# Optimization experiments

Hardware: AMD Instinct MI355X
Metric: run time of the kernel (lower is better)

Reference implementation:

```python
import jax, jax.numpy as jnp
import numpy as np

N_NODES = 50000
N_EDGES = 500000
NEG_SLOPE = 0.2


def gat_conv(h, src, dst, W, attn_l, attn_r, bias, activation):
    """DGL-style GATConv (feat_drop=attn_drop=0, no residual).
    h: [N, F_in]; W: [F_in, H*D]; attn_l/attn_r: [H, D]; bias: [H*D].
    Returns [N, H, D]."""
    H, D = attn_l.shape
    feat = (h @ W).reshape(-1, H, D)                      # [N, H, D]
    el = (feat * attn_l).sum(-1)                          # [N, H]
    er = (feat * attn_r).sum(-1)                          # [N, H]
    e = jax.nn.leaky_relu(el[src] + er[dst], NEG_SLOPE)   # [E, H] edge logits
    # edge softmax over incoming edges of each dst node
    emax = jax.ops.segment_max(e, dst, num_segments=N_NODES)
    emax = jnp.where(jnp.isfinite(emax), emax, 0.0)       # guard zero in-degree
    ee = jnp.exp(e - emax[dst])                           # [E, H]
    denom = jax.ops.segment_sum(ee, dst, num_segments=N_NODES)
    alpha = ee / jnp.maximum(denom[dst], 1e-9)            # [E, H]
    # weighted scatter-aggregate of source features
    out = jax.ops.segment_sum(feat[src] * alpha[..., None], dst,
                              num_segments=N_NODES)       # [N, H, D]
    out = out + bias.reshape(1, H, D)
    return activation(out) if activation is not None else out


def setup_inputs() -> dict:
    key = jax.random.key(0)
    ks = jax.random.split(key, 20)
    in0, in1, hid, heads, ncls = 256, 128, 64, 8, 10

    def xn(k, shape):
        fan = shape[0] + (shape[1] if len(shape) > 1 else shape[0])
        return jax.random.normal(k, shape, jnp.float32) * np.float32(np.sqrt(2.0 / fan)) * 1.414

    inp = {
        "feat0": jax.random.normal(ks[0], (30000, in0), jnp.float32),
        "feat1": jax.random.normal(ks[1], (20000, in1), jnp.float32),
        "fc0_w": xn(ks[2], (in0, hid)), "fc0_b": jnp.zeros((hid,), jnp.float32),
        "fc1_w": xn(ks[3], (in1, hid)), "fc1_b": jnp.zeros((hid,), jnp.float32),
        "W0": xn(ks[4], (hid, heads * hid)),
        "al0": xn(ks[5], (heads, hid)), "ar0": xn(ks[6], (heads, hid)),
        "b0": jnp.zeros((heads * hid,), jnp.float32),
        "W1": xn(ks[7], (heads * hid, heads * hid)),
        "al1": xn(ks[8], (heads, hid)), "ar1": xn(ks[9], (heads, hid)),
        "b1": jnp.zeros((heads * hid,), jnp.float32),
        "W2": xn(ks[10], (heads * hid, 1 * ncls)),
        "al2": xn(ks[11], (1, ncls)), "ar2": xn(ks[12], (1, ncls)),
        "b2": jnp.zeros((ncls,), jnp.float32),
        "edge_index": jax.random.randint(ks[13], (2, N_EDGES), 0, N_NODES, jnp.int64
                                         if jax.config.jax_enable_x64 else jnp.int32),
    }
    return inp


def reference(feat0, feat1, fc0_w, fc0_b, fc1_w, fc1_b,
              W0, al0, ar0, b0, W1, al1, ar1, b1, W2, al2, ar2, b2,
              edge_index):
    src, dst = edge_index[0], edge_index[1]
    # per-type linear projection then concat along node axis
    h = jnp.concatenate([feat0 @ fc0_w + fc0_b, feat1 @ fc1_w + fc1_b], axis=0)
    h = gat_conv(h, src, dst, W0, al0, ar0, b0, jax.nn.elu).reshape(N_NODES, -1)
    h = gat_conv(h, src, dst, W1, al1, ar1, b1, jax.nn.elu).reshape(N_NODES, -1)
    logits = gat_conv(h, src, dst, W2, al2, ar2, b2, None).mean(axis=1)  # [N, ncls]
    return logits
```

## Files before the change

kernel.cpp:

```cpp
#include <hip/hip_runtime.h>
#include <hip/hip_bf16.h>
#include <hip/hip_fp16.h>

#define N_NODES 50000
#define N_EDGES 500000
#define HEADS 8
#define HID 64
#define HD 512
#define NCLS 10
#define M_PAD 50048

typedef _Float16 f16x8 __attribute__((ext_vector_type(8)));
typedef _Float16 h8v   __attribute__((ext_vector_type(8)));
typedef float    f32x4 __attribute__((ext_vector_type(4)));

#define GLD_LDS16(g, l) __builtin_amdgcn_global_load_lds( \
    (__attribute__((address_space(1))) void*)(g),         \
    (__attribute__((address_space(3))) void*)(l), 16, 0, 0)

#define T0_TILES 469
#define T1_TILES 313
__global__ __launch_bounds__(256) void fc_gemm(const float* __restrict__ A0,
                                               const float* __restrict__ B0,
                                               const float* __restrict__ bias0,
                                               const float* __restrict__ A1,
                                               const float* __restrict__ B1,
                                               const float* __restrict__ bias1,
                                               _Float16* __restrict__ Cb) {
    __shared__ float As[16][68];
    __shared__ float Bs[16][68];
    int bid = blockIdx.x;
    const float* A; const float* B; const float* bias;
    int M, K, row_off, m0;
    if (bid < T0_TILES) { A = A0; B = B0; bias = bias0; M = 30000; K = 256; row_off = 0;     m0 = bid * 64; }
    else                { A = A1; B = B1; bias = bias1; M = 20000; K = 128; row_off = 30000; m0 = (bid - T0_TILES) * 64; }
    int tid = threadIdx.x;
    int tx = tid & 15, ty = tid >> 4;
    float acc[4][4] = {};
    int arow = tid >> 2;
    int akq  = (tid & 3) * 4;
    int brow = tid >> 4;
    int bcol = (tid & 15) * 4;
    for (int k0 = 0; k0 < K; k0 += 16) {
        int m = m0 + arow;
        float4 av = make_float4(0.f, 0.f, 0.f, 0.f);
        if (m < M) av = *(const float4*)(A + (size_t)m * K + k0 + akq);
        As[akq + 0][arow] = av.x; As[akq + 1][arow] = av.y;
        As[akq + 2][arow] = av.z; As[akq + 3][arow] = av.w;
        float4 bv = *(const float4*)(B + (size_t)(k0 + brow) * 64 + bcol);
        *(float4*)(&Bs[brow][bcol]) = bv;
        __syncthreads();
#pragma unroll
        for (int k = 0; k < 16; k++) {
            float4 a = *(const float4*)(&As[k][ty * 4]);
            float4 b = *(const float4*)(&Bs[k][tx * 4]);
            float av4[4] = {a.x, a.y, a.z, a.w};
            float bv4[4] = {b.x, b.y, b.z, b.w};
#pragma unroll
            for (int i = 0; i < 4; i++)
#pragma unroll
                for (int j = 0; j < 4; j++) acc[i][j] += av4[i] * bv4[j];
        }
        __syncthreads();
    }
#pragma unroll
    for (int i = 0; i < 4; i++) {
        int m = m0 + ty * 4 + i;
        if (m < M) {
#pragma unroll
            for (int j = 0; j < 4; j++) {
                int col = tx * 4 + j;
                Cb[(size_t)(row_off + m) * 64 + col] = (_Float16)(acc[i][j] + bias[col]);
            }
        }
    }
}

#define NBLK_SCAN 196

__global__ void count_kernel(const int* __restrict__ dst, int* __restrict__ cnt) {
    int t = blockIdx.x * blockDim.x + threadIdx.x;
    if (t < N_EDGES) atomicAdd(&cnt[dst[t]], 1);
}

__global__ void scan_part(const int* __restrict__ cnt, int* __restrict__ part) {
    __shared__ int s[256];
    int i = blockIdx.x * 256 + threadIdx.x;
    s[threadIdx.x] = (i < N_NODES) ? cnt[i] : 0;
    __syncthreads();
    for (int off = 128; off; off >>= 1) {
        if (threadIdx.x < off) s[threadIdx.x] += s[threadIdx.x + off];
        __syncthreads();
    }
    if (threadIdx.x == 0) part[blockIdx.x] = s[0];
}

__global__ void scan_offs(int* __restrict__ part) {
    __shared__ int s[256];
    int tid = threadIdx.x;
    int v = (tid < NBLK_SCAN) ? part[tid] : 0;
    s[tid] = v;
    __syncthreads();
    for (int off = 1; off < 256; off <<= 1) {
        int x = (tid >= off) ? s[tid - off] : 0;
        __syncthreads();
        s[tid] += x;
        __syncthreads();
    }
    if (tid < NBLK_SCAN) part[tid] = s[tid] - v;
}

__global__ void scan_apply(const int* __restrict__ cnt, const int* __restrict__ part,
                           int* __restrict__ rp, int* __restrict__ cur) {
    __shared__ int s[256];
    int tid = threadIdx.x;
    int i = blockIdx.x * 256 + tid;
    int v = (i < N_NODES) ? cnt[i] : 0;
    s[tid] = v;
    __syncthreads();
    for (int off = 1; off < 256; off <<= 1) {
        int x = (tid >= off) ? s[tid - off] : 0;
        __syncthreads();
        s[tid] += x;
        __syncthreads();
    }
    if (i < N_NODES) {
        int excl = s[tid] - v + part[blockIdx.x];
        rp[i] = excl; cur[i] = excl;
    }
    if (i == 0) rp[N_NODES] = N_EDGES;
}

__global__ void scatter_kernel(const int* __restrict__ src, const int* __restrict__ dst,
                               int* __restrict__ cursor, int* __restrict__ src_sorted) {
    int t = blockIdx.x * blockDim.x + threadIdx.x;
    if (t >= N_EDGES) return;
    int pos = atomicAdd(&cursor[dst[t]], 1);
    src_sorted[pos] = src[t];
}

__global__ void wtrans(const float* __restrict__ W0, const float* __restrict__ W1,
                       _Float16* __restrict__ W0t, _Float16* __restrict__ W1t) {
    int t = blockIdx.x * blockDim.x + threadIdx.x;
    if (t < 64 * 512) {
        int n = t >> 6, k = t & 63;
        W0t[t] = (_Float16)W0[k * 512 + n];
    } else {
        int u = t - 64 * 512;
        if (u >= 512 * 512) return;
        int n = u >> 9, k = u & 511;
        W1t[u] = (_Float16)W1[k * 512 + n];
    }
}

__global__ __launch_bounds__(256) void gemm_mfma(const _Float16* __restrict__ A,
                                                 const _Float16* __restrict__ Bt,
                                                 _Float16* __restrict__ Cb,
                                                 const float* __restrict__ al,
                                                 const float* __restrict__ ar,
                                                 float* __restrict__ el,
                                                 float* __restrict__ er,
                                                 int M, int N, int K) {
    __shared__ _Float16 Asl[128 * 32];
    __shared__ _Float16 Bsl[128 * 32];
    int t = threadIdx.x;
    int m0 = blockIdx.y * 128, n0 = blockIdx.x * 128;
    int lane = t & 63;
    int w = t >> 6;
    int wm = (w & 1) * 64, wn = (w >> 1) * 64;
    int l15 = lane & 15, quad = lane >> 4;
    f32x4 acc[4][4];
#pragma unroll
    for (int i = 0; i < 4; i++)
#pragma unroll
        for (int j = 0; j < 4; j++) acc[i][j] = (f32x4){0.f, 0.f, 0.f, 0.f};

    int fb0 = t * 16;
    int fb1 = fb0 + 4096;
    int row0 = fb0 >> 6, kg0 = ((fb0 >> 4) & 3) ^ (row0 & 3);
    int row1 = fb1 >> 6, kg1 = ((fb1 >> 4) & 3) ^ (row1 & 3);

    for (int k0 = 0; k0 < K; k0 += 32) {
        GLD_LDS16(A + (size_t)(m0 + row0) * K + k0 + kg0 * 8, (char*)Asl + fb0);
        GLD_LDS16(A + (size_t)(m0 + row1) * K + k0 + kg1 * 8, (char*)Asl + fb1);
        GLD_LDS16(Bt + (size_t)(n0 + row0) * K + k0 + kg0 * 8, (char*)Bsl + fb0);
        GLD_LDS16(Bt + (size_t)(n0 + row1) * K + k0 + kg1 * 8, (char*)Bsl + fb1);
        __syncthreads();
        f16x8 af[4], bfr[4];
#pragma unroll
        for (int i = 0; i < 4; i++) {
            int r = wm + i * 16 + l15;
            int kg = quad ^ (r & 3);
            af[i] = *(const f16x8*)(Asl + r * 32 + kg * 8);
        }
#pragma unroll
        for (int j = 0; j < 4; j++) {
            int r = wn + j * 16 + l15;
            int kg = quad ^ (r & 3);
            bfr[j] = *(const f16x8*)(Bsl + r * 32 + kg * 8);
        }
#pragma unroll
        for (int i = 0; i < 4; i++)
#pragma unroll
            for (int j = 0; j < 4; j++)
                acc[i][j] = __builtin_amdgcn_mfma_f32_16x16x32_f16(af[i], bfr[j], acc[i][j], 0, 0, 0);
        __syncthreads();
    }
#pragma unroll
    for (int i = 0; i < 4; i++) {
        int rbase = m0 + wm + i * 16 + quad * 4;
#pragma unroll
        for (int j = 0; j < 4; j++) {
            int col = n0 + wn + j * 16 + l15;
#pragma unroll
            for (int r = 0; r < 4; r++) {
                int row = rbase + r;
                if (row < M) Cb[(size_t)row * N + col] = (_Float16)acc[i][j][r];
            }
        }
    }
    int h = (n0 + wn) >> 6;
    float alv[4], arv[4];
#pragma unroll
    for (int j = 0; j < 4; j++) {
        alv[j] = al[h * 64 + j * 16 + l15];
        arv[j] = ar[h * 64 + j * 16 + l15];
    }
#pragma unroll
    for (int i = 0; i < 4; i++) {
#pragma unroll
        for (int r = 0; r < 4; r++) {
            float sl = 0.f, sr = 0.f;
#pragma unroll
            for (int j = 0; j < 4; j++) {
                float v = acc[i][j][r];
                sl += v * alv[j]; sr += v * arv[j];
            }
#pragma unroll
            for (int mk = 1; mk < 16; mk <<= 1) {
                sl += __shfl_xor(sl, mk);
                sr += __shfl_xor(sr, mk);
            }
            int row = m0 + wm + i * 16 + quad * 4 + r;
            if (l15 == 0 && row < M) {
                el[row * HEADS + h] = sl;
                er[row * HEADS + h] = sr;
            }
        }
    }
}

__global__ __launch_bounds__(256) void attn_agg(
        const int* __restrict__ rp, const int* __restrict__ srcs,
        const float* __restrict__ el, const float* __restrict__ er,
        const _Float16* __restrict__ feat, const float* __restrict__ bias,
        _Float16* __restrict__ out) {
    __shared__ float aS[4][592];
    __shared__ int   sS[4][64];
    int lane = threadIdx.x & 63;
    int w    = threadIdx.x >> 6;
    int n    = blockIdx.x * 4 + w;
    int s0 = rp[n], s1 = rp[n + 1];
    int deg = s1 - s0;
    float er8[8];
    {
        f32x4 a = *(const f32x4*)(er + (size_t)n * 8);
        f32x4 b = *(const f32x4*)(er + (size_t)n * 8 + 4);
        er8[0]=a[0]; er8[1]=a[1]; er8[2]=a[2]; er8[3]=a[3];
        er8[4]=b[0]; er8[5]=b[1]; er8[6]=b[2]; er8[7]=b[3];
    }
    bool fast = (deg <= 64);
    if (fast) {
        bool act = lane < deg;
        int sp = act ? srcs[s0 + lane] : 0;
        sS[w][lane] = sp;
        f32x4 ea = {0.f,0.f,0.f,0.f}, eb = {0.f,0.f,0.f,0.f};
        if (act) {
            ea = *(const f32x4*)(el + (size_t)sp * 8);
            eb = *(const f32x4*)(el + (size_t)sp * 8 + 4);
        }
        float e8[8] = {ea[0],ea[1],ea[2],ea[3],eb[0],eb[1],eb[2],eb[3]};
#pragma unroll
        for (int h = 0; h < 8; h++) {
            float e = e8[h] + er8[h];
            e = e > 0.f ? e : 0.2f * e;
            e8[h] = act ? e : -1e30f;
        }
#pragma unroll
        for (int h = 0; h < 8; h++) {
            float mm = e8[h];
#pragma unroll
            for (int mk = 1; mk < 64; mk <<= 1) mm = fmaxf(mm, __shfl_xor(mm, mk));
            float pv = act ? __expf(e8[h] - mm) : 0.f;
            float ss = pv;
#pragma unroll
            for (int mk = 1; mk < 64; mk <<= 1) ss += __shfl_xor(ss, mk);
            aS[w][lane * 9 + h] = pv * (1.f / fmaxf(ss, 1e-9f));
        }
    } else {
        float m8[8], s8[8];
#pragma unroll
        for (int h = 0; h < 8; h++) { m8[h] = -1e30f; s8[h] = 0.f; }
        for (int base = s0; base < s1; base += 64) {
            bool act = base + lane < s1;
            int sp = act ? srcs[base + lane] : 0;
            f32x4 ea = {0.f,0.f,0.f,0.f}, eb = {0.f,0.f,0.f,0.f};
            if (act) {
                ea = *(const f32x4*)(el + (size_t)sp * 8);
                eb = *(const f32x4*)(el + (size_t)sp * 8 + 4);
            }
            float ev[8] = {ea[0],ea[1],ea[2],ea[3],eb[0],eb[1],eb[2],eb[3]};
#pragma unroll
            for (int h = 0; h < 8; h++) {
                float e = ev[h] + er8[h];
                e = e > 0.f ? e : 0.2f * e;
                e = act ? e : -1e30f;
                float cm = e;
#pragma unroll
                for (int mk = 1; mk < 64; mk <<= 1) cm = fmaxf(cm, __shfl_xor(cm, mk));
                float nm = fmaxf(m8[h], cm);
                float pv = act ? __expf(e - nm) : 0.f;
#pragma unroll
                for (int mk = 1; mk < 64; mk <<= 1) pv += __shfl_xor(pv, mk);
                s8[h] = s8[h] * __expf(m8[h] - nm) + pv;
                m8[h] = nm;
            }
        }
        if (lane == 0) {
#pragma unroll
            for (int h = 0; h < 8; h++) {
                aS[w][576 + h] = 1.f / fmaxf(s8[h], 1e-9f);
                aS[w][584 + h] = m8[h];
            }
        }
    }
    __builtin_amdgcn_wave_barrier();
    int hh = lane >> 3, d0 = (lane & 7) * 8;
    h8v acc8a = {(_Float16)0, (_Float16)0, (_Float16)0, (_Float16)0,
                 (_Float16)0, (_Float16)0, (_Float16)0, (_Float16)0};
    h8v acc8b = acc8a;
    const _Float16* colbase = feat + hh * 64 + d0;
    if (fast) {
        int p = 0;
        for (; p + 2 <= deg; p += 2) {
            int spa = sS[w][p], spb = sS[w][p + 1];
            _Float16 aa = (_Float16)aS[w][p * 9 + hh];
            _Float16 ab = (_Float16)aS[w][(p + 1) * 9 + hh];
            h8v a8a = {aa, aa, aa, aa, aa, aa, aa, aa};
            h8v a8b = {ab, ab, ab, ab, ab, ab, ab, ab};
            h8v fa = *(const h8v*)(colbase + (size_t)spa * HD);
            h8v fb = *(const h8v*)(colbase + (size_t)spb * HD);
            acc8a += a8a * fa;
            acc8b += a8b * fb;
        }
        if (p < deg) {
            int sp = sS[w][p];
            _Float16 ah = (_Float16)aS[w][p * 9 + hh];
            h8v a8 = {ah, ah, ah, ah, ah, ah, ah, ah};
            h8v f = *(const h8v*)(colbase + (size_t)sp * HD);
            acc8a += a8 * f;
        }
    } else {
        float inv_l = aS[w][576 + hh];
        float m_l   = aS[w][584 + hh];
        float ern_l = er[(size_t)n * 8 + hh];
        for (int p = s0; p < s1; p++) {
            int sp = srcs[p];
            float e = el[(size_t)sp * 8 + hh] + ern_l;
            e = e > 0.f ? e : 0.2f * e;
            _Float16 ah = (_Float16)(__expf(e - m_l) * inv_l);
            h8v a8 = {ah, ah, ah, ah, ah, ah, ah, ah};
            h8v f = *(const h8v*)(colbase + (size_t)sp * HD);
            acc8a += a8 * f;
        }
    }
    acc8a += acc8b;
    float4 b0v = *(const float4*)(bias + lane * 8);
    float4 b1v = *(const float4*)(bias + lane * 8 + 4);
    float bb[8] = {b0v.x,b0v.y,b0v.z,b0v.w,b1v.x,b1v.y,b1v.z,b1v.w};
    h8v o;
#pragma unroll
    for (int j = 0; j < 8; j++) {
        float x = (float)acc8a[j] + bb[j];
        x = x > 0.f ? x : __expf(x) - 1.f;
        o[j] = (_Float16)x;
    }
    *(h8v*)(out + (size_t)n * HD + lane * 8) = o;
}

__global__ __launch_bounds__(256) void gemm_n10v2(
        const _Float16* __restrict__ A, const float* __restrict__ B,
        const float* __restrict__ al2, const float* __restrict__ ar2,
        float* __restrict__ C, float* __restrict__ el, float* __restrict__ er) {
    __shared__ float Bs[512 * 11];
    int t = threadIdx.x;
    for (int i = t; i < 512 * NCLS; i += 256) {
        int k = i / NCLS, c = i - k * NCLS;
        Bs[k * 11 + c] = B[i];
    }
    __syncthreads();
    int lane = t & 63;
    int m = blockIdx.x * 4 + (t >> 6);
    float acc[NCLS];
#pragma unroll
    for (int c = 0; c < NCLS; c++) acc[c] = 0.f;
    const _Float16* a = A + (size_t)m * HD;
#pragma unroll
    for (int j = 0; j < 8; j++) {
        float av = (float)a[j * 64 + lane];
        const float* br = Bs + (j * 64 + lane) * 11;
#pragma unroll
        for (int c = 0; c < NCLS; c++) acc[c] += av * br[c];
    }
#pragma unroll
    for (int c = 0; c < NCLS; c++)
#pragma unroll
        for (int mk = 1; mk < 64; mk <<= 1) acc[c] += __shfl_xor(acc[c], mk);
    if (lane == 0) {
        float e1 = 0.f, e2 = 0.f;
#pragma unroll
        for (int c = 0; c < NCLS; c++) { e1 += acc[c] * al2[c]; e2 += acc[c] * ar2[c]; }
        el[m] = e1; er[m] = e2;
#pragma unroll
        for (int c = 0; c < NCLS; c++) C[(size_t)m * NCLS + c] = acc[c];
    }
}

__global__ __launch_bounds__(256) void attn2_agg2(
        const int* __restrict__ rp, const int* __restrict__ srcs,
        const float* __restrict__ el, const float* __restrict__ er,
        const float* __restrict__ feat2, const float* __restrict__ b2,
        float* __restrict__ out) {
    int lane = threadIdx.x & 63;
    int n = blockIdx.x * 4 + (threadIdx.x >> 6);
    int s0 = rp[n], s1 = rp[n + 1], deg = s1 - s0;
    float ern = er[n];
    float facc[NCLS];
#pragma unroll
    for (int c = 0; c < NCLS; c++) facc[c] = 0.f;
    if (deg <= 64) {
        bool act = lane < deg;
        int sp = act ? srcs[s0 + lane] : 0;
        float e = act ? el[sp] + ern : 0.f;
        e = e > 0.f ? e : 0.2f * e;
        if (!act) e = -1e30f;
        float mm = e;
#pragma unroll
        for (int mk = 1; mk < 64; mk <<= 1) mm = fmaxf(mm, __shfl_xor(mm, mk));
        float pv = act ? __expf(e - mm) : 0.f;
        float ss = pv;
#pragma unroll
        for (int mk = 1; mk < 64; mk <<= 1) ss += __shfl_xor(ss, mk);
        float a = pv / fmaxf(ss, 1e-9f);
        if (act) {
#pragma unroll
            for (int c = 0; c < NCLS; c++) facc[c] = a * feat2[(size_t)sp * NCLS + c];
        }
    } else {
        float mm = -1e30f, ssum = 0.f;
        for (int base = s0; base < s1; base += 64) {
            bool act = base + lane < s1;
            int sp = act ? srcs[base + lane] : 0;
            float e = act ? el[sp] + ern : 0.f;
            e = e > 0.f ? e : 0.2f * e;
            if (!act) e = -1e30f;
            float cm = e;
#pragma unroll
            for (int mk = 1; mk < 64; mk <<= 1) cm = fmaxf(cm, __shfl_xor(cm, mk));
            float nm = fmaxf(mm, cm);
            float pv = act ? __expf(e - nm) : 0.f;
#pragma unroll
            for (int mk = 1; mk < 64; mk <<= 1) pv += __shfl_xor(pv, mk);
            ssum = ssum * __expf(mm - nm) + pv;
            mm = nm;
        }
        float inv = 1.f / fmaxf(ssum, 1e-9f);
        for (int base = s0; base < s1; base += 64) {
            bool act = base + lane < s1;
            int sp = act ? srcs[base + lane] : 0;
            float e = act ? el[sp] + ern : 0.f;
            e = e > 0.f ? e : 0.2f * e;
            float a = act ? __expf(e - mm) * inv : 0.f;
            if (act) {
#pragma unroll
                for (int c = 0; c < NCLS; c++) facc[c] += a * feat2[(size_t)sp * NCLS + c];
            }
        }
    }
#pragma unroll
    for (int c = 0; c < NCLS; c++)
#pragma unroll
        for (int mk = 1; mk < 64; mk <<= 1) facc[c] += __shfl_xor(facc[c], mk);
    if (lane == 0) {
#pragma unroll
        for (int c = 0; c < NCLS; c++) out[(size_t)n * NCLS + c] = facc[c] + b2[c];
    }
}

extern "C" void kernel_launch(void* const* d_in, const int* in_sizes, int n_in,
                              void* d_out, int out_size, void* d_ws, size_t ws_size,
                              hipStream_t stream) {
    const float* feat0 = (const float*)d_in[0];
    const float* feat1 = (const float*)d_in[1];
    const float* fc0_w = (const float*)d_in[2];
    const float* fc0_b = (const float*)d_in[3];
    const float* fc1_w = (const float*)d_in[4];
    const float* fc1_b = (const float*)d_in[5];
    const float* W0    = (const float*)d_in[6];
    const float* al0   = (const float*)d_in[7];
    const float* ar0   = (const float*)d_in[8];
    const float* b0    = (const float*)d_in[9];
    const float* W1    = (const float*)d_in[10];
    const float* al1   = (const float*)d_in[11];
    const float* ar1   = (const float*)d_in[12];
    const float* b1    = (const float*)d_in[13];
    const float* W2    = (const float*)d_in[14];
    const float* al2   = (const float*)d_in[15];
    const float* ar2   = (const float*)d_in[16];
    const float* b2    = (const float*)d_in[17];
    const int* eidx    = (const int*)d_in[18];
    const int* src = eidx;
    const int* dst = eidx + N_EDGES;
    float* out = (float*)d_out;

    char* ws = (char*)d_ws;
    size_t off = 0;
    auto alloc = [&](size_t bytes) { size_t o = off; off = (off + bytes + 255) & ~(size_t)255; return o; };

    _Float16* featA = (_Float16*)(ws + alloc((size_t)M_PAD * HD * 2));
    _Float16* aggh  = (_Float16*)(ws + alloc((size_t)M_PAD * HD * 2));
    _Float16* h0h   = (_Float16*)(ws + alloc((size_t)M_PAD * 64 * 2));
    float*    feat2 = (float*)(ws + alloc((size_t)N_NODES * NCLS * 4));
    float*    el    = (float*)(ws + alloc((size_t)N_NODES * HEADS * 4));
    float*    er    = (float*)(ws + alloc((size_t)N_NODES * HEADS * 4));
    float*    el2   = (float*)(ws + alloc((size_t)N_NODES * 4));
    float*    er2   = (float*)(ws + alloc((size_t)N_NODES * 4));
    int*      cnt   = (int*)  (ws + alloc((size_t)N_NODES * 4));
    int*      rp    = (int*)  (ws + alloc((size_t)(N_NODES + 1) * 4));
    int*      cur   = (int*)  (ws + alloc((size_t)N_NODES * 4));
    int*      srcs  = (int*)  (ws + alloc((size_t)N_EDGES * 4));
    int*      part  = (int*)  (ws + alloc(1024));
    _Float16* W0t   = (_Float16*)(ws + alloc(512 * 64 * 2));
    _Float16* W1t   = (_Float16*)(ws + alloc(512 * 512 * 2));

    fc_gemm<<<T0_TILES + T1_TILES, 256, 0, stream>>>(feat0, fc0_w, fc0_b,
                                                     feat1, fc1_w, fc1_b, h0h);
    wtrans<<<(64 * 512 + 512 * 512 + 255) / 256, 256, 0, stream>>>(W0, W1, W0t, W1t);

    hipMemsetAsync(cnt, 0, N_NODES * sizeof(int), stream);
    count_kernel<<<(N_EDGES + 255) / 256, 256, 0, stream>>>(dst, cnt);
    scan_part<<<NBLK_SCAN, 256, 0, stream>>>(cnt, part);
    scan_offs<<<1, 256, 0, stream>>>(part);
    scan_apply<<<NBLK_SCAN, 256, 0, stream>>>(cnt, part, rp, cur);
    scatter_kernel<<<(N_EDGES + 255) / 256, 256, 0, stream>>>(src, dst, cur, srcs);

    dim3 ggrid(HD / 128, M_PAD / 128);

    gemm_mfma<<<ggrid, 256, 0, stream>>>(h0h, W0t, featA, al0, ar0, el, er,
                                         N_NODES, HD, 64);
    attn_agg<<<N_NODES / 4, 256, 0, stream>>>(rp, srcs, el, er, featA, b0, aggh);

    gemm_mfma<<<ggrid, 256, 0, stream>>>(aggh, W1t, featA, al1, ar1, el, er,
                                         N_NODES, HD, HD);
    attn_agg<<<N_NODES / 4, 256, 0, stream>>>(rp, srcs, el, er, featA, b1, aggh);

    gemm_n10v2<<<N_NODES / 4, 256, 0, stream>>>(aggh, W2, al2, ar2, feat2, el2, er2);
    attn2_agg2<<<N_NODES / 4, 256, 0, stream>>>(rp, srcs, el2, er2, feat2, b2, out);
}
```

Baseline: 544.3 us.

## Widen GEMM tile to 128x256 with XCD-aware block mapping and unroll aggregation by 4

The projection GEMM now uses 512-thread blocks covering 128 rows by 256 columns, so each A tile is loaded once per two column halves instead of four times. It uses a 1D grid remapped so that consecutive groups of 8 blocks share row tiles, which is meant to improve L2 locality across XCDs. The attention aggregation fast path is unrolled to four independent gathers and accumulators to expose more memory-level parallelism. The wider block raises register and LDS use per block and may lower occupancy.

```diff
diff --git a/kernel.cpp b/kernel.cpp
--- a/kernel.cpp
+++ b/kernel.cpp
@@ -9,6 +9,7 @@
 #define HD 512
 #define NCLS 10
 #define M_PAD 50048
+#define YTILES 391
 
 typedef _Float16 f16x8 __attribute__((ext_vector_type(8)));
 typedef _Float16 h8v   __attribute__((ext_vector_type(8)));
@@ -153,18 +154,23 @@
     }
 }
 
-__global__ __launch_bounds__(256) void gemm_mfma(const _Float16* __restrict__ A,
-                                                 const _Float16* __restrict__ Bt,
-                                                 _Float16* __restrict__ Cb,
-                                                 const float* __restrict__ al,
-                                                 const float* __restrict__ ar,
-                                                 float* __restrict__ el,
-                                                 float* __restrict__ er,
-                                                 int M, int N, int K) {
+__global__ __launch_bounds__(512) void gemm_mfma_wide(const _Float16* __restrict__ A,
+                                                      const _Float16* __restrict__ Bt,
+                                                      _Float16* __restrict__ Cb,
+                                                      const float* __restrict__ al,
+                                                      const float* __restrict__ ar,
+                                                      float* __restrict__ el,
+                                                      float* __restrict__ er,
+                                                      int M, int K) {
     __shared__ _Float16 Asl[128 * 32];
-    __shared__ _Float16 Bsl[128 * 32];
+    __shared__ _Float16 Bsl[256 * 32];
+    int bid = blockIdx.x;
+    int k8 = bid & 7, jj = bid >> 3;
+    int y = k8 + 8 * (jj >> 1);
+    if (y >= YTILES) return;
+    int m0 = y * 128;
+    int n0 = (jj & 1) * 256;
     int t = threadIdx.x;
-    int m0 = blockIdx.y * 128, n0 = blockIdx.x * 128;
     int lane = t & 63;
     int w = t >> 6;
     int wm = (w & 1) * 64, wn = (w >> 1) * 64;
@@ -175,16 +181,17 @@
 #pragma unroll
         for (int j = 0; j < 4; j++) acc[i][j] = (f32x4){0.f, 0.f, 0.f, 0.f};
 
-    int fb0 = t * 16;
-    int fb1 = fb0 + 4096;
-    int row0 = fb0 >> 6, kg0 = ((fb0 >> 4) & 3) ^ (row0 & 3);
-    int row1 = fb1 >> 6, kg1 = ((fb1 >> 4) & 3) ^ (row1 & 3);
+    int fbA = t * 16;
+    int rowA = fbA >> 6, kgA = ((fbA >> 4) & 3) ^ (rowA & 3);
+    int fbB0 = t * 16;
+    int fbB1 = fbB0 + 8192;
+    int rowB0 = fbB0 >> 6, kgB0 = ((fbB0 >> 4) & 3) ^ (rowB0 & 3);
+    int rowB1 = fbB1 >> 6, kgB1 = ((fbB1 >> 4) & 3) ^ (rowB1 & 3);
 
     for (int k0 = 0; k0 < K; k0 += 32) {
-        GLD_LDS16(A + (size_t)(m0 + row0) * K + k0 + kg0 * 8, (char*)Asl + fb0);
-        GLD_LDS16(A + (size_t)(m0 + row1) * K + k0 + kg1 * 8, (char*)Asl + fb1);
-        GLD_LDS16(Bt + (size_t)(n0 + row0) * K + k0 + kg0 * 8, (char*)Bsl + fb0);
-        GLD_LDS16(Bt + (size_t)(n0 + row1) * K + k0 + kg1 * 8, (char*)Bsl + fb1);
+        GLD_LDS16(A + (size_t)(m0 + rowA) * K + k0 + kgA * 8, (char*)Asl + fbA);
+        GLD_LDS16(Bt + (size_t)(n0 + rowB0) * K + k0 + kgB0 * 8, (char*)Bsl + fbB0);
+        GLD_LDS16(Bt + (size_t)(n0 + rowB1) * K + k0 + kgB1 * 8, (char*)Bsl + fbB1);
         __syncthreads();
         f16x8 af[4], bfr[4];
 #pragma unroll
@@ -215,7 +222,7 @@
 #pragma unroll
             for (int r = 0; r < 4; r++) {
                 int row = rbase + r;
-                if (row < M) Cb[(size_t)row * N + col] = (_Float16)acc[i][j][r];
+                if (row < M) Cb[(size_t)row * HD + col] = (_Float16)acc[i][j][r];
             }
         }
     }
@@ -336,29 +343,38 @@
     }
     __builtin_amdgcn_wave_barrier();
     int hh = lane >> 3, d0 = (lane & 7) * 8;
-    h8v acc8a = {(_Float16)0, (_Float16)0, (_Float16)0, (_Float16)0,
-                 (_Float16)0, (_Float16)0, (_Float16)0, (_Float16)0};
-    h8v acc8b = acc8a;
+    h8v z = {(_Float16)0, (_Float16)0, (_Float16)0, (_Float16)0,
+             (_Float16)0, (_Float16)0, (_Float16)0, (_Float16)0};
+    h8v acc0 = z, acc1 = z, acc2 = z, acc3 = z;
     const _Float16* colbase = feat + hh * 64 + d0;
     if (fast) {
         int p = 0;
-        for (; p + 2 <= deg; p += 2) {
-            int spa = sS[w][p], spb = sS[w][p + 1];
+        for (; p + 4 <= deg; p += 4) {
+            int spa = sS[w][p],     spb = sS[w][p + 1];
+            int spc = sS[w][p + 2], spd = sS[w][p + 3];
             _Float16 aa = (_Float16)aS[w][p * 9 + hh];
             _Float16 ab = (_Float16)aS[w][(p + 1) * 9 + hh];
+            _Float16 ac = (_Float16)aS[w][(p + 2) * 9 + hh];
+            _Float16 ad = (_Float16)aS[w][(p + 3) * 9 + hh];
+            h8v fa = *(const h8v*)(colbase + (size_t)spa * HD);
+            h8v fb = *(const h8v*)(colbase + (size_t)spb * HD);
+            h8v fc = *(const h8v*)(colbase + (size_t)spc * HD);
+            h8v fd = *(const h8v*)(colbase + (size_t)spd * HD);
             h8v a8a = {aa, aa, aa, aa, aa, aa, aa, aa};
             h8v a8b = {ab, ab, ab, ab, ab, ab, ab, ab};
-            h8v fa = *(const h8v*)(colbase + (size_t)spa * HD);
-            h8v fb = *(const h8v*)(colbase + (size_t)spb * HD);
-            acc8a += a8a * fa;
-            acc8b += a8b * fb;
-        }
-        if (p < deg) {
+            h8v a8c = {ac, ac, ac, ac, ac, ac, ac, ac};
+            h8v a8d = {ad, ad, ad, ad, ad, ad, ad, ad};
+            acc0 += a8a * fa;
+            acc1 += a8b * fb;
+            acc2 += a8c * fc;
+            acc3 += a8d * fd;
+        }
+        for (; p < deg; p++) {
             int sp = sS[w][p];
             _Float16 ah = (_Float16)aS[w][p * 9 + hh];
             h8v a8 = {ah, ah, ah, ah, ah, ah, ah, ah};
             h8v f = *(const h8v*)(colbase + (size_t)sp * HD);
-            acc8a += a8 * f;
+            acc0 += a8 * f;
         }
     } else {
         float inv_l = aS[w][576 + hh];
@@ -371,17 +387,17 @@
             _Float16 ah = (_Float16)(__expf(e - m_l) * inv_l);
             h8v a8 = {ah, ah, ah, ah, ah, ah, ah, ah};
             h8v f = *(const h8v*)(colbase + (size_t)sp * HD);
-            acc8a += a8 * f;
-        }
-    }
-    acc8a += acc8b;
+            acc0 += a8 * f;
+        }
+    }
+    acc0 += acc1; acc2 += acc3; acc0 += acc2;
     float4 b0v = *(const float4*)(bias + lane * 8);
     float4 b1v = *(const float4*)(bias + lane * 8 + 4);
     float bb[8] = {b0v.x,b0v.y,b0v.z,b0v.w,b1v.x,b1v.y,b1v.z,b1v.w};
     h8v o;
 #pragma unroll
     for (int j = 0; j < 8; j++) {
-        float x = (float)acc8a[j] + bb[j];
+        float x = (float)acc0[j] + bb[j];
         x = x > 0.f ? x : __expf(x) - 1.f;
         o[j] = (_Float16)x;
     }
@@ -554,14 +570,14 @@
     scan_apply<<<NBLK_SCAN, 256, 0, stream>>>(cnt, part, rp, cur);
     scatter_kernel<<<(N_EDGES + 255) / 256, 256, 0, stream>>>(src, dst, cur, srcs);
 
-    dim3 ggrid(HD / 128, M_PAD / 128);
-
-    gemm_mfma<<<ggrid, 256, 0, stream>>>(h0h, W0t, featA, al0, ar0, el, er,
-                                         N_NODES, HD, 64);
+    int ggrid = 8 * 98;
+
+    gemm_mfma_wide<<<ggrid, 512, 0, stream>>>(h0h, W0t, featA, al0, ar0, el, er,
+                                              N_NODES, 64);
     attn_agg<<<N_NODES / 4, 256, 0, stream>>>(rp, srcs, el, er, featA, b0, aggh);
 
-    gemm_mfma<<<ggrid, 256, 0, stream>>>(aggh, W1t, featA, al1, ar1, el, er,
-                                         N_NODES, HD, HD);
+    gemm_mfma_wide<<<ggrid, 512, 0, stream>>>(aggh, W1t, featA, al1, ar1, el, er,
+                                              N_NODES, HD);
     attn_agg<<<N_NODES / 4, 256, 0, stream>>>(rp, srcs, el, er, featA, b1, aggh);
 
     gemm_n10v2<<<N_NODES / 4, 256, 0, stream>>>(aggh, W2, al2, ar2, feat2, el2, er2);
```

New measurement: 535.8 us. About the same (-1.6%).
